# Optimization experiments

Hardware: AMD Instinct MI355X
Metric: run time of the kernel (lower is better)

Reference implementation:

```python
import jax, jax.numpy as jnp
import numpy as np

D_MODEL = 1024
N_HEADS = 16
HEAD_DIM = D_MODEL // N_HEADS
B, L, E = 2, 2048, 256


def _linear_params(key, d_out, d_in):
    kw, kb = jax.random.split(key)
    lim = 1.0 / np.sqrt(d_in)
    W = jax.random.uniform(kw, (d_out, d_in), jnp.float32, -lim, lim)
    b = jax.random.uniform(kb, (d_out,), jnp.float32, -lim, lim)
    return W, b


def setup_inputs() -> dict:
    key = jax.random.key(0)
    ks = jax.random.split(key, 10)
    x = jax.random.normal(ks[0], (B, L, D_MODEL), jnp.float32)
    kg_embeds = jax.random.normal(ks[1], (B, E, D_MODEL), jnp.float32)
    Wq, bq = _linear_params(ks[2], D_MODEL, D_MODEL)
    Wk, bk = _linear_params(ks[3], D_MODEL, D_MODEL)
    Wv, bv = _linear_params(ks[4], D_MODEL, D_MODEL)
    Wo, bo = _linear_params(ks[5], D_MODEL, D_MODEL)
    Wkk, bkk = _linear_params(ks[6], D_MODEL, D_MODEL)
    Wkv, bkv = _linear_params(ks[7], D_MODEL, D_MODEL)
    Wg, bg = _linear_params(ks[8], D_MODEL, 2 * D_MODEL)
    return {"x": x, "kg_embeds": kg_embeds,
            "Wq": Wq, "bq": bq, "Wk": Wk, "bk": bk, "Wv": Wv, "bv": bv,
            "Wkk": Wkk, "bkk": bkk, "Wkv": Wkv, "bkv": bkv,
            "Wo": Wo, "bo": bo, "Wg": Wg, "bg": bg}


def _heads(t):
    # [B, S, D] -> [B, H, S, hd]
    Bb, S, _ = t.shape
    return t.reshape(Bb, S, N_HEADS, HEAD_DIM).transpose(0, 2, 1, 3)


def reference(x, kg_embeds, Wq, bq, Wk, bk, Wv, bv, Wkk, bkk, Wkv, bkv, Wo, bo, Wg, bg):
    scale = HEAD_DIM ** -0.5
    q = _heads(x @ Wq.T + bq)                      # [B,H,L,hd]
    k = _heads(x @ Wk.T + bk)
    v = _heads(x @ Wv.T + bv)
    k_kg = _heads(kg_embeds @ Wkk.T + bkk)         # [B,H,E,hd]
    v_kg = _heads(kg_embeds @ Wkv.T + bkv)
    k_aug = jnp.concatenate([k, k_kg], axis=2)     # [B,H,L+E,hd]
    v_aug = jnp.concatenate([v, v_kg], axis=2)
    scores = jnp.einsum('bhld,bhmd->bhlm', q, k_aug) * scale  # [B,H,L,L+E]
    attn = jax.nn.softmax(scores, axis=-1)
    out = jnp.einsum('bhlm,bhmd->bhld', attn, v_aug)           # [B,H,L,hd]
    out = out.transpose(0, 2, 1, 3).reshape(x.shape)            # [B,L,D]
    kg_global = jnp.broadcast_to(kg_embeds.mean(axis=1, keepdims=True), x.shape)
    gate = jax.nn.sigmoid(jnp.concatenate([out, kg_global], axis=-1) @ Wg.T + bg)
    return gate * (out @ Wo.T + bo) + (1.0 - gate) * x
```

## Files before the change

### kernel.cpp

```cpp
#include <hip/hip_runtime.h>
#include <stdint.h>

typedef unsigned short ushort_t;
typedef __attribute__((ext_vector_type(8))) short short8;
typedef __attribute__((ext_vector_type(4))) short short4v;
typedef __attribute__((ext_vector_type(4))) float f32x4;
typedef __attribute__((ext_vector_type(4))) unsigned uintx4;

#define DEV static __device__ __forceinline__

DEV unsigned short f2bf(float f) {
  unsigned u = __builtin_bit_cast(unsigned, f);
  u += 0x7fffu + ((u >> 16) & 1u);
  return (unsigned short)(u >> 16);
}
DEV float bf2f(unsigned short b) {
  return __builtin_bit_cast(float, (unsigned)b << 16);
}

DEV void gl16(const void* g, void* l) {
  __builtin_amdgcn_global_load_lds(
      (__attribute__((address_space(1))) char*)(unsigned long long)g,
      (__attribute__((address_space(3))) char*)(unsigned)(unsigned long long)l,
      16, 0, 0);
}

DEV f32x4 mfma_bf16(short8 a, short8 b, f32x4 c) {
  return __builtin_amdgcn_mfma_f32_16x16x32_bf16(a, b, c, 0, 0, 0);
}

DEV unsigned cvtpk(float lo, float hi) {
  unsigned r;
  asm("v_cvt_pk_bf16_f32 %0, %1, %2" : "=v"(r) : "v"(lo), "v"(hi));
  return r;
}
DEV void swap_net(unsigned& a, unsigned& b) {
  asm("v_permlane32_swap_b32 %0, %1" : "+v"(a), "+v"(b));
  asm("v_permlane16_swap_b32 %0, %1" : "+v"(a), "+v"(b));
}
DEV float redmax4(float x) {
  unsigned a = __builtin_bit_cast(unsigned, x), b = a;
  asm("v_permlane16_swap_b32 %0, %1" : "+v"(a), "+v"(b));
  float y = fmaxf(__builtin_bit_cast(float, a), __builtin_bit_cast(float, b));
  unsigned c = __builtin_bit_cast(unsigned, y), d = c;
  asm("v_permlane32_swap_b32 %0, %1" : "+v"(c), "+v"(d));
  return fmaxf(__builtin_bit_cast(float, c), __builtin_bit_cast(float, d));
}
DEV float lanebcast(float v, int srclane) {
  return __builtin_bit_cast(float,
      __builtin_amdgcn_ds_bpermute(srclane * 4, __builtin_bit_cast(int, v)));
}

__global__ __launch_bounds__(256) void k_cvt_all(
    const float* __restrict__ x, const float* __restrict__ kg,
    const float* __restrict__ Wq, const float* __restrict__ Wk, const float* __restrict__ Wv,
    const float* __restrict__ Wkk, const float* __restrict__ Wkv,
    const float* __restrict__ Wo, const float* __restrict__ Wg,
    ushort_t* __restrict__ xh, ushort_t* __restrict__ kgh,
    ushort_t* __restrict__ WB1, ushort_t* __restrict__ WB2, ushort_t* __restrict__ WB3) {
  const int b = blockIdx.x;
  if (b >= 10752) {
    const int i = (b - 10752) * 256 + threadIdx.x;
    const int r = i >> 8, c = (i & 255) * 4;
    const float4 v = *(const float4*)(Wg + (size_t)r * 2048 + c);
    short4v o;
    o.x = (short)f2bf(v.x); o.y = (short)f2bf(v.y); o.z = (short)f2bf(v.z); o.w = (short)f2bf(v.w);
    *(short4v*)(WB3 + 1048576 + (size_t)r * 1024 + c) = o;
    return;
  }
  const float* src;
  ushort_t* dst;
  int off;
  if (b < 4096)       { src = x;   dst = xh;            off = b; }
  else if (b < 4608)  { src = kg;  dst = kgh;           off = b - 4096; }
  else if (b < 5632)  { src = Wq;  dst = WB1;           off = b - 4608; }
  else if (b < 6656)  { src = Wk;  dst = WB1 + 1048576; off = b - 5632; }
  else if (b < 7680)  { src = Wv;  dst = WB1 + 2097152; off = b - 6656; }
  else if (b < 8704)  { src = Wkk; dst = WB2;           off = b - 7680; }
  else if (b < 9728)  { src = Wkv; dst = WB2 + 1048576; off = b - 8704; }
  else                { src = Wo;  dst = WB3;           off = b - 9728; }
  const int i = off * 1024 + threadIdx.x * 4;
  const float4 v = *(const float4*)(src + i);
  short4v o;
  o.x = (short)f2bf(v.x); o.y = (short)f2bf(v.y); o.z = (short)f2bf(v.z); o.w = (short)f2bf(v.w);
  *(short4v*)(dst + i) = o;
}

__global__ __launch_bounds__(256) void k_kgmean(const float* __restrict__ kg, float* __restrict__ out) {
  const int i = blockIdx.x * 256 + threadIdx.x;
  const int b = i >> 10, d = i & 1023;
  float s = 0.f;
  #pragma unroll 4
  for (int e = 0; e < 256; e++) s += kg[((size_t)b * 256 + e) * 1024 + d];
  out[i] = s * (1.0f / 256.0f);
}

__global__ __launch_bounds__(256) void k_g2(const float* __restrict__ kgm, const float* __restrict__ Wg,
                                            const float* __restrict__ bg, float* __restrict__ g2) {
  const int w = threadIdx.x >> 6, l = threadIdx.x & 63;
  const int idx = blockIdx.x * 4 + w;
  const int b = idx >> 10, n = idx & 1023;
  const float* wr = Wg + (size_t)n * 2048 + 1024;
  const float* mb = kgm + b * 1024;
  float s = 0.f;
  #pragma unroll
  for (int j = 0; j < 16; j++) s += mb[j * 64 + l] * wr[j * 64 + l];
  #pragma unroll
  for (int m = 32; m >= 1; m >>= 1) s += __shfl_xor(s, m);
  if (l == 0) g2[idx] = s + bg[n];
}

template <int MODE>
__global__ __launch_bounds__(256, 3) void k_mm128(
    const ushort_t* __restrict__ A0, const ushort_t* __restrict__ B0,
    const ushort_t* __restrict__ A1, const ushort_t* __restrict__ B1,
    const float* __restrict__ f0, const float* __restrict__ f1, const float* __restrict__ f2,
    const float* __restrict__ f3, const float* __restrict__ f4,
    ushort_t* __restrict__ o0, ushort_t* __restrict__ o1, ushort_t* __restrict__ o2) {
  __shared__ __align__(16) char SHb[49152];
  const int tid = threadIdx.x;
  const int w = tid >> 6, l = tid & 63;
  const int wr = w >> 1, wc = w & 1;
  const int fr = l & 15, fg = l >> 4;

  int m0, n0, iskg = 0;
  if (MODE == 0) {
    const int wg = ((int)blockIdx.x & 7) * 104 + ((int)blockIdx.x >> 3);
    if (wg < 768) { m0 = (wg / 24) * 128; n0 = (wg % 24) * 128; }
    else          { const int k = wg - 768; iskg = 1; m0 = (k >> 4) * 128; n0 = (k & 15) * 128; }
  } else {
    const int wg = ((int)blockIdx.x & 7) * 64 + ((int)blockIdx.x >> 3);
    m0 = (wg >> 4) * 128; n0 = (wg & 15) * 128;
  }
  const ushort_t* A = (MODE == 0 && iskg) ? A1 : A0;
  const ushort_t* B = (MODE == 0 && iskg) ? B1 : B0;

  int grow[2], gcb[2];
  #pragma unroll
  for (int j = 0; j < 2; j++) {
    const int beta = j * 256 + tid;
    const int rp = beta >> 3;
    const int u = (beta & 7) ^ (rp & 7);
    grow[j] = 2 * rp + (u >> 2);
    gcb[j] = u & 3;
  }
  const char* gA[2];
  const char* gB[2];
  #pragma unroll
  for (int j = 0; j < 2; j++) {
    gA[j] = (const char*)A + (size_t)(m0 + grow[j]) * 2048 + gcb[j] * 16;
    gB[j] = (const char*)B + (size_t)(n0 + grow[j]) * 2048 + gcb[j] * 16;
  }

  auto stage = [&](int s, int kt) {
    char* As = SHb + s * 16384;
    char* Bs = As + 8192;
    const int ko = kt * 64;
    #pragma unroll
    for (int j = 0; j < 2; j++) {
      gl16(gA[j] + ko, As + j * 4096 + tid * 16);
      gl16(gB[j] + ko, Bs + j * 4096 + tid * 16);
    }
  };

  int aoff[4], boff[4];
  #pragma unroll
  for (int i = 0; i < 4; i++) {
    const int rowa = wr * 64 + i * 16 + fr;
    aoff[i] = (rowa >> 1) * 128 + ((((rowa & 1) << 6) | (fg << 4)) ^ (((rowa >> 1) & 7) << 4));
    const int rowb = wc * 64 + i * 16 + fr;
    boff[i] = (rowb >> 1) * 128 + ((((rowb & 1) << 6) | (fg << 4)) ^ (((rowb >> 1) & 7) << 4));
  }

  f32x4 acc[4][4] = {};

  stage(0, 0);
  stage(1, 1);
  int sc = 0, sn2 = 2;
  for (int kt = 0; kt < 32; kt++) {
    if (kt < 31) asm volatile("s_waitcnt vmcnt(4)" ::: "memory");
    else         asm volatile("s_waitcnt vmcnt(0)" ::: "memory");
    __builtin_amdgcn_s_barrier();
    asm volatile("" ::: "memory");
    if (kt < 30) stage(sn2, kt + 2);
    const char* Ab = SHb + sc * 16384;
    const char* Bb = Ab + 8192;
    short8 af[4], bf[4];
    #pragma unroll
    for (int j = 0; j < 4; j++) bf[j] = *(const short8*)(Bb + boff[j]);
    #pragma unroll
    for (int i = 0; i < 4; i++) af[i] = *(const short8*)(Ab + aoff[i]);
    __builtin_amdgcn_s_setprio(1);
    #pragma unroll
    for (int i = 0; i < 4; i++)
      #pragma unroll
      for (int j = 0; j < 4; j++)
        acc[i][j] = mfma_bf16(af[i], bf[j], acc[i][j]);
    __builtin_amdgcn_s_setprio(0);
    sc++; if (sc == 3) sc = 0;
    sn2++; if (sn2 == 3) sn2 = 0;
  }
  __syncthreads();

  const int sec = n0 >> 10;
  const bool isV = (MODE == 0) && ((!iskg && sec == 2) || (iskg && sec == 1));

  if (isV) {
    ushort_t* SHs = (ushort_t*)SHb;
    const float* bV = iskg ? f4 : f2;
    const int bidx = iskg ? (m0 >> 8) : (m0 >> 11);
    const int colbase = iskg ? (2048 + (m0 & 255)) : (m0 & 2047);
    #pragma unroll
    for (int i = 0; i < 4; i++) {
      #pragma unroll
      for (int j = 0; j < 4; j++) {
        const int nl = wc * 64 + j * 16 + fr;
        const int ml0 = wr * 64 + i * 16 + fg * 4;
        const float bb = bV[(n0 & 1023) + nl];
        short4v pk;
        #pragma unroll
        for (int r = 0; r < 4; r++) pk[r] = (short)f2bf(acc[i][j][r] + bb);
        *(short4v*)(SHs + nl * 128 + (ml0 ^ ((nl & 7) << 3))) = pk;
      }
    }
    __syncthreads();
    const int row = tid >> 1, half = tid & 1;
    const int h = ((n0 & 1023) >> 6) + (row >> 6);
    const int d = row & 63;
    ushort_t* dst = o2 + ((size_t)(bidx * 16 + h) * 64 + d) * 2304 + colbase + half * 64;
    const ushort_t* srow2 = SHs + row * 128;
    #pragma unroll
    for (int k2 = 0; k2 < 8; k2++) {
      const int me = (half * 64 + k2 * 8) ^ ((row & 7) << 3);
      *(short8*)(dst + k2 * 8) = *(const short8*)(srow2 + me);
    }
    return;
  }

  #pragma unroll
  for (int i = 0; i < 4; i++) {
    #pragma unroll
    for (int j = 0; j < 4; j++) {
      const int nn = (n0 & 1023) + wc * 64 + j * 16 + fr;
      const int h = nn >> 6, d = nn & 63;
      #pragma unroll
      for (int r = 0; r < 4; r++) {
        const int m = m0 + wr * 64 + i * 16 + fg * 4 + r;
        const float v = acc[i][j][r];
        if (MODE == 0) {
          if (iskg) {
            const int b = m >> 8, e = m & 255;
            o1[((size_t)(b * 16 + h) * 2304 + 2048 + e) * 64 + d] = f2bf(v + f3[nn]);
          } else if (sec == 0) {
            const int b = m >> 11, lq = m & 2047;
            o0[((size_t)(b * 16 + h) * 2048 + lq) * 64 + d] = f2bf((v + f0[nn]) * 0.18033688f);
          } else {
            const int b = m >> 11, lq = m & 2047;
            o1[((size_t)(b * 16 + h) * 2304 + lq) * 64 + d] = f2bf(v + f1[nn]);
          }
        } else {
          if (sec == 0) o0[(size_t)m * 1024 + nn] = f2bf(v + f0[nn]);
          else          o1[(size_t)m * 1024 + nn] = f2bf(v + f1[(m >> 11) * 1024 + nn]);
        }
      }
    }
  }
}

__global__ __launch_bounds__(256, 4) void k_attn(
    const ushort_t* __restrict__ Qg, const ushort_t* __restrict__ Kg,
    const ushort_t* __restrict__ Vtg, ushort_t* __restrict__ Og) {
  __shared__ __align__(16) ushort_t Ks[2][64 * 64];
  __shared__ __align__(16) ushort_t Vs[2][64 * 64];
  const int tid = threadIdx.x;
  const int w = tid >> 6, l = tid & 63;
  const int fr = l & 15, fg = l >> 4;

  const int id = blockIdx.y * gridDim.x + blockIdx.x;
  const int bh = (id & 7) * 4 + ((id >> 3) >> 5);
  const int q0 = ((id >> 3) & 31) * 64 + w * 16;

  short8 qf[2];
  {
    const short* qrow = (const short*)(Qg + ((size_t)bh * 2048 + q0 + fr) * 64);
    qf[0] = *(const short8*)(qrow + fg * 8);
    qf[1] = *(const short8*)(qrow + 32 + fg * 8);
  }

  constexpr short ONE = 0x3F80;
  const short8 ones = {ONE, ONE, ONE, ONE, ONE, ONE, ONE, ONE};

  f32x4 o[4] = {};
  f32x4 lacc = {};
  float mrun = -1.0e30f;

  const int rsub = tid >> 3;
  const int cS = ((tid & 7) * 16) ^ ((rsub & 7) << 4);
  const char* kbase = (const char*)(Kg + (size_t)bh * 2304 * 64);
  const char* vbase = (const char*)(Vtg + (size_t)bh * 64 * 2304);

  auto stage = [&](int nb, int tile) {
    #pragma unroll
    for (int j = 0; j < 2; j++) {
      const int row = j * 32 + rsub;
      gl16(kbase + (size_t)(tile * 64 + row) * 128 + cS,
           (char*)&Ks[nb][0] + j * 4096 + tid * 16);
      gl16(vbase + (size_t)row * 4608 + tile * 128 + cS,
           (char*)&Vs[nb][0] + j * 4096 + tid * 16);
    }
  };

  stage(0, 0);

  const int rswz = (fr & 7) << 4;

  for (int mt = 0; mt < 36; mt++) {
    __syncthreads();
    if (mt < 35) stage((mt + 1) & 1, mt + 1);

    const char* Kb = (const char*)&Ks[mt & 1][0];
    const char* Vb = (const char*)&Vs[mt & 1][0];

    f32x4 s[4];
    #pragma unroll
    for (int t = 0; t < 4; t++) {
      const int rb = (t * 16 + fr) * 128 + fg * 16;
      const short8 k0 = *(const short8*)(Kb + (rb ^ rswz));
      const short8 k1 = *(const short8*)(Kb + ((rb + 64) ^ rswz));
      f32x4 z = {};
      z = mfma_bf16(k0, qf[0], z);
      z = mfma_bf16(k1, qf[1], z);
      s[t] = z;
    }

    float m = s[0][0];
    #pragma unroll
    for (int t = 0; t < 4; t++)
      #pragma unroll
      for (int r = 0; r < 4; r++) m = fmaxf(m, s[t][r]);
    const float mx = redmax4(m);
    if (__any(mx - mrun > 11.5416f)) {
      const float mn = fmaxf(mrun, mx);
      const float al = __builtin_amdgcn_exp2f(mrun - mn);
      mrun = mn;
      float ab[4];
      #pragma unroll
      for (int r = 0; r < 4; r++) ab[r] = lanebcast(al, fg * 4 + r);
      #pragma unroll
      for (int r = 0; r < 4; r++) {
        lacc[r] *= ab[r];
        #pragma unroll
        for (int dt = 0; dt < 4; dt++) o[dt][r] *= ab[r];
      }
    }
    #pragma unroll
    for (int t = 0; t < 4; t++)
      #pragma unroll
      for (int r = 0; r < 4; r++)
        s[t][r] = __builtin_amdgcn_exp2f(s[t][r] - mrun);

    #pragma unroll
    for (int c = 0; c < 2; c++) {
      unsigned a0 = cvtpk(s[2 * c][0], s[2 * c][1]);
      unsigned b0 = cvtpk(s[2 * c + 1][0], s[2 * c + 1][1]);
      unsigned a1 = cvtpk(s[2 * c][2], s[2 * c][3]);
      unsigned b1 = cvtpk(s[2 * c + 1][2], s[2 * c + 1][3]);
      swap_net(a0, b0);
      swap_net(a1, b1);
      uintx4 u;
      u.x = a0; u.y = a1; u.z = b0; u.w = b1;
      const short8 pf = __builtin_bit_cast(short8, u);
      lacc = mfma_bf16(pf, ones, lacc);
      #pragma unroll
      for (int dt = 0; dt < 4; dt++) {
        const int vb2 = ((dt * 16 + fr) * 128) + fg * 16 + c * 64;
        const short8 vf = *(const short8*)(Vb + (vb2 ^ rswz));
        o[dt] = mfma_bf16(pf, vf, o[dt]);
      }
    }
  }

  const int b = bh >> 4, h = bh & 15;
  #pragma unroll
  for (int r = 0; r < 4; r++) {
    const float inv = 1.0f / lacc[r];
    const int q = q0 + fg * 4 + r;
    ushort_t* orow = Og + ((size_t)b * 2048 + q) * 1024 + h * 64;
    #pragma unroll
    for (int dt = 0; dt < 4; dt++) orow[dt * 16 + fr] = f2bf(o[dt][r] * inv);
  }
}

__global__ __launch_bounds__(256) void k_final(const float* __restrict__ x,
                                               const ushort_t* __restrict__ OUT,
                                               const ushort_t* __restrict__ GL,
                                               float* __restrict__ y) {
  const int i = (blockIdx.x * 256 + threadIdx.x) * 4;
  const float4 xv = *(const float4*)(x + i);
  const short4v ov = *(const short4v*)((const short*)OUT + i);
  const short4v gv = *(const short4v*)((const short*)GL + i);
  float4 r;
  {
    const float o0 = bf2f((unsigned short)ov.x);
    const float g0 = 1.f / (1.f + __expf(-bf2f((unsigned short)gv.x)));
    r.x = xv.x + g0 * (o0 - xv.x);
  }
  {
    const float o1 = bf2f((unsigned short)ov.y);
    const float g1 = 1.f / (1.f + __expf(-bf2f((unsigned short)gv.y)));
    r.y = xv.y + g1 * (o1 - xv.y);
  }
  {
    const float o2 = bf2f((unsigned short)ov.z);
    const float g2 = 1.f / (1.f + __expf(-bf2f((unsigned short)gv.z)));
    r.z = xv.z + g2 * (o2 - xv.z);
  }
  {
    const float o3 = bf2f((unsigned short)ov.w);
    const float g3 = 1.f / (1.f + __expf(-bf2f((unsigned short)gv.w)));
    r.w = xv.w + g3 * (o3 - xv.w);
  }
  *(float4*)(y + i) = r;
}

extern "C" void kernel_launch(void* const* d_in, const int* in_sizes, int n_in,
                              void* d_out, int out_size, void* d_ws, size_t ws_size,
                              hipStream_t stream) {
  (void)in_sizes; (void)n_in; (void)out_size; (void)ws_size;
  const float* x   = (const float*)d_in[0];
  const float* kg  = (const float*)d_in[1];
  const float* Wq  = (const float*)d_in[2];
  const float* bq  = (const float*)d_in[3];
  const float* Wk  = (const float*)d_in[4];
  const float* bk  = (const float*)d_in[5];
  const float* Wv  = (const float*)d_in[6];
  const float* bv  = (const float*)d_in[7];
  const float* Wkk = (const float*)d_in[8];
  const float* bkk = (const float*)d_in[9];
  const float* Wkv = (const float*)d_in[10];
  const float* bkv = (const float*)d_in[11];
  const float* Wo  = (const float*)d_in[12];
  const float* bo  = (const float*)d_in[13];
  const float* Wg  = (const float*)d_in[14];
  const float* bg  = (const float*)d_in[15];
  float* y = (float*)d_out;

  char* ws = (char*)d_ws;
  size_t off = 0;
  auto take = [&](size_t bytes) {
    char* p = ws + off;
    off += (bytes + 255) & ~(size_t)255;
    return p;
  };
  ushort_t* xh   = (ushort_t*)take((size_t)4096 * 1024 * 2);
  ushort_t* kgh  = (ushort_t*)take((size_t)512 * 1024 * 2);
  ushort_t* WB1  = (ushort_t*)take((size_t)3072 * 1024 * 2);
  ushort_t* WB2  = (ushort_t*)take((size_t)2048 * 1024 * 2);
  ushort_t* WB3  = (ushort_t*)take((size_t)2048 * 1024 * 2);
  ushort_t* Qg   = (ushort_t*)take((size_t)32 * 2048 * 64 * 2);
  ushort_t* Kaug = (ushort_t*)take((size_t)32 * 2304 * 64 * 2);
  ushort_t* Vt   = (ushort_t*)take((size_t)32 * 2304 * 64 * 2);
  ushort_t* Og   = (ushort_t*)take((size_t)4096 * 1024 * 2);
  ushort_t* OUTb = (ushort_t*)take((size_t)4096 * 1024 * 2);
  ushort_t* GLb  = (ushort_t*)take((size_t)4096 * 1024 * 2);
  float* kgm     = (float*)take(2048 * 4);
  float* g2      = (float*)take(2048 * 4);

  k_cvt_all<<<11776, 256, 0, stream>>>(x, kg, Wq, Wk, Wv, Wkk, Wkv, Wo, Wg,
                                       xh, kgh, WB1, WB2, WB3);
  k_kgmean<<<8, 256, 0, stream>>>(kg, kgm);
  k_g2<<<512, 256, 0, stream>>>(kgm, Wg, bg, g2);

  k_mm128<0><<<832, 256, 0, stream>>>(xh, WB1, kgh, WB2,
                                      bq, bk, bv, bkk, bkv, Qg, Kaug, Vt);
  k_attn<<<dim3(32, 32), 256, 0, stream>>>(Qg, Kaug, Vt, Og);
  k_mm128<1><<<512, 256, 0, stream>>>(Og, WB3, nullptr, nullptr,
                                      bo, g2, nullptr, nullptr, nullptr, OUTb, GLb, nullptr);
  k_final<<<4096, 256, 0, stream>>>(x, OUTb, GLb, y);
}
```

Before: 179.4 us.

## Fuse output and gate GEMMs with the sigmoid-blend epilogue into one kernel

Adds a dedicated output GEMM kernel in which each block computes a 64x128 tile against both Wo and the gate weights at once, sharing the A tile. The sigmoid gating and residual blend with x are applied in the epilogue and written straight to y. This drops the final elementwise kernel and the bf16 OUT/GL intermediate round trips through memory. The cost is more accumulator registers (occupancy target lowered to 2), plus a small reordering of the max reduction in attention.

```diff
diff --git a/kernel.cpp b/kernel.cpp
--- a/kernel.cpp
+++ b/kernel.cpp
@@ -110,7 +110,6 @@
   if (l == 0) g2[idx] = s + bg[n];
 }
 
-template <int MODE>
 __global__ __launch_bounds__(256, 3) void k_mm128(
     const ushort_t* __restrict__ A0, const ushort_t* __restrict__ B0,
     const ushort_t* __restrict__ A1, const ushort_t* __restrict__ B1,
@@ -124,16 +123,13 @@
   const int fr = l & 15, fg = l >> 4;
 
   int m0, n0, iskg = 0;
-  if (MODE == 0) {
+  {
     const int wg = ((int)blockIdx.x & 7) * 104 + ((int)blockIdx.x >> 3);
     if (wg < 768) { m0 = (wg / 24) * 128; n0 = (wg % 24) * 128; }
     else          { const int k = wg - 768; iskg = 1; m0 = (k >> 4) * 128; n0 = (k & 15) * 128; }
-  } else {
-    const int wg = ((int)blockIdx.x & 7) * 64 + ((int)blockIdx.x >> 3);
-    m0 = (wg >> 4) * 128; n0 = (wg & 15) * 128;
-  }
-  const ushort_t* A = (MODE == 0 && iskg) ? A1 : A0;
-  const ushort_t* B = (MODE == 0 && iskg) ? B1 : B0;
+  }
+  const ushort_t* A = iskg ? A1 : A0;
+  const ushort_t* B = iskg ? B1 : B0;
 
   int grow[2], gcb[2];
   #pragma unroll
@@ -203,7 +199,7 @@
   __syncthreads();
 
   const int sec = n0 >> 10;
-  const bool isV = (MODE == 0) && ((!iskg && sec == 2) || (iskg && sec == 1));
+  const bool isV = (!iskg && sec == 2) || (iskg && sec == 1);
 
   if (isV) {
     ushort_t* SHs = (ushort_t*)SHb;
@@ -247,21 +243,126 @@
       for (int r = 0; r < 4; r++) {
         const int m = m0 + wr * 64 + i * 16 + fg * 4 + r;
         const float v = acc[i][j][r];
-        if (MODE == 0) {
-          if (iskg) {
-            const int b = m >> 8, e = m & 255;
-            o1[((size_t)(b * 16 + h) * 2304 + 2048 + e) * 64 + d] = f2bf(v + f3[nn]);
-          } else if (sec == 0) {
-            const int b = m >> 11, lq = m & 2047;
-            o0[((size_t)(b * 16 + h) * 2048 + lq) * 64 + d] = f2bf((v + f0[nn]) * 0.18033688f);
-          } else {
-            const int b = m >> 11, lq = m & 2047;
-            o1[((size_t)(b * 16 + h) * 2304 + lq) * 64 + d] = f2bf(v + f1[nn]);
-          }
+        if (iskg) {
+          const int b = m >> 8, e = m & 255;
+          o1[((size_t)(b * 16 + h) * 2304 + 2048 + e) * 64 + d] = f2bf(v + f3[nn]);
+        } else if (sec == 0) {
+          const int b = m >> 11, lq = m & 2047;
+          o0[((size_t)(b * 16 + h) * 2048 + lq) * 64 + d] = f2bf((v + f0[nn]) * 0.18033688f);
         } else {
-          if (sec == 0) o0[(size_t)m * 1024 + nn] = f2bf(v + f0[nn]);
-          else          o1[(size_t)m * 1024 + nn] = f2bf(v + f1[(m >> 11) * 1024 + nn]);
+          const int b = m >> 11, lq = m & 2047;
+          o1[((size_t)(b * 16 + h) * 2304 + lq) * 64 + d] = f2bf(v + f1[nn]);
         }
+      }
+    }
+  }
+}
+
+__global__ __launch_bounds__(256, 2) void k_mmout(
+    const ushort_t* __restrict__ Og, const ushort_t* __restrict__ WB3,
+    const float* __restrict__ bo, const float* __restrict__ g2v,
+    const float* __restrict__ x, float* __restrict__ y) {
+  __shared__ __align__(16) char SHb[61440];
+  const int tid = threadIdx.x;
+  const int w = tid >> 6, l = tid & 63;
+  const int wr = w >> 1, wc = w & 1;
+  const int fr = l & 15, fg = l >> 4;
+
+  const int wg = ((int)blockIdx.x & 7) * 64 + ((int)blockIdx.x >> 3);
+  const int m0 = (wg >> 3) * 64, n0 = (wg & 7) * 128;
+
+  const int rpA = tid >> 3, uA = (tid & 7) ^ (rpA & 7);
+  const char* gAp = (const char*)Og + (size_t)(m0 + 2 * rpA + (uA >> 2)) * 2048 + (uA & 3) * 16;
+  int grow[2], gcb[2];
+  #pragma unroll
+  for (int j = 0; j < 2; j++) {
+    const int beta = j * 256 + tid;
+    const int rp = beta >> 3;
+    const int u = (beta & 7) ^ (rp & 7);
+    grow[j] = 2 * rp + (u >> 2);
+    gcb[j] = u & 3;
+  }
+  const char* gBo[2];
+  const char* gBg[2];
+  #pragma unroll
+  for (int j = 0; j < 2; j++) {
+    gBo[j] = (const char*)WB3 + (size_t)(n0 + grow[j]) * 2048 + gcb[j] * 16;
+    gBg[j] = (const char*)(WB3 + 1048576) + (size_t)(n0 + grow[j]) * 2048 + gcb[j] * 16;
+  }
+
+  auto stage = [&](int s, int kt) {
+    char* As = SHb + s * 20480;
+    const int ko = kt * 64;
+    gl16(gAp + ko, As + tid * 16);
+    #pragma unroll
+    for (int j = 0; j < 2; j++) {
+      gl16(gBo[j] + ko, As + 4096 + j * 4096 + tid * 16);
+      gl16(gBg[j] + ko, As + 12288 + j * 4096 + tid * 16);
+    }
+  };
+
+  int aoff[2], boff[4];
+  #pragma unroll
+  for (int i = 0; i < 2; i++) {
+    const int rowa = wr * 32 + i * 16 + fr;
+    aoff[i] = (rowa >> 1) * 128 + ((((rowa & 1) << 6) | (fg << 4)) ^ (((rowa >> 1) & 7) << 4));
+  }
+  #pragma unroll
+  for (int j = 0; j < 4; j++) {
+    const int rowb = wc * 64 + j * 16 + fr;
+    boff[j] = (rowb >> 1) * 128 + ((((rowb & 1) << 6) | (fg << 4)) ^ (((rowb >> 1) & 7) << 4));
+  }
+
+  f32x4 ao[2][4] = {};
+  f32x4 ag[2][4] = {};
+
+  stage(0, 0);
+  stage(1, 1);
+  int sc = 0, sn2 = 2;
+  for (int kt = 0; kt < 32; kt++) {
+    if (kt < 31) asm volatile("s_waitcnt vmcnt(5)" ::: "memory");
+    else         asm volatile("s_waitcnt vmcnt(0)" ::: "memory");
+    __builtin_amdgcn_s_barrier();
+    asm volatile("" ::: "memory");
+    if (kt < 30) stage(sn2, kt + 2);
+    const char* Ab = SHb + sc * 20480;
+    short8 af[2], bof[4], bgf[4];
+    #pragma unroll
+    for (int i = 0; i < 2; i++) af[i] = *(const short8*)(Ab + aoff[i]);
+    #pragma unroll
+    for (int j = 0; j < 4; j++) {
+      bof[j] = *(const short8*)(Ab + 4096 + boff[j]);
+      bgf[j] = *(const short8*)(Ab + 12288 + boff[j]);
+    }
+    __builtin_amdgcn_s_setprio(1);
+    #pragma unroll
+    for (int i = 0; i < 2; i++)
+      #pragma unroll
+      for (int j = 0; j < 4; j++) {
+        ao[i][j] = mfma_bf16(af[i], bof[j], ao[i][j]);
+        ag[i][j] = mfma_bf16(af[i], bgf[j], ag[i][j]);
+      }
+    __builtin_amdgcn_s_setprio(0);
+    sc++; if (sc == 3) sc = 0;
+    sn2++; if (sn2 == 3) sn2 = 0;
+  }
+
+  const int bidx = m0 >> 11;
+  #pragma unroll
+  for (int i = 0; i < 2; i++) {
+    #pragma unroll
+    for (int j = 0; j < 4; j++) {
+      const int nn = n0 + wc * 64 + j * 16 + fr;
+      const float bb = bo[nn];
+      const float gg = g2v[bidx * 1024 + nn];
+      #pragma unroll
+      for (int r = 0; r < 4; r++) {
+        const int m = m0 + wr * 32 + i * 16 + fg * 4 + r;
+        const float co = ao[i][j][r] + bb;
+        const float cg = ag[i][j][r] + gg;
+        const float gate = 1.0f / (1.0f + __builtin_amdgcn_exp2f(cg * -1.4426950408889634f));
+        const float xv = x[(size_t)m * 1024 + nn];
+        y[(size_t)m * 1024 + nn] = xv + gate * (co - xv);
       }
     }
   }
@@ -333,11 +434,14 @@
       s[t] = z;
     }
 
-    float m = s[0][0];
-    #pragma unroll
-    for (int t = 0; t < 4; t++)
-      #pragma unroll
-      for (int r = 0; r < 4; r++) m = fmaxf(m, s[t][r]);
+    float m = fmaxf(s[0][0], s[0][1]);
+    m = fmaxf(fmaxf(m, s[0][2]), s[0][3]);
+    m = fmaxf(fmaxf(m, s[1][0]), s[1][1]);
+    m = fmaxf(fmaxf(m, s[1][2]), s[1][3]);
+    m = fmaxf(fmaxf(m, s[2][0]), s[2][1]);
+    m = fmaxf(fmaxf(m, s[2][2]), s[2][3]);
+    m = fmaxf(fmaxf(m, s[3][0]), s[3][1]);
+    m = fmaxf(fmaxf(m, s[3][2]), s[3][3]);
     const float mx = redmax4(m);
     if (__any(mx - mrun > 11.5416f)) {
       const float mn = fmaxf(mrun, mx);
@@ -389,38 +493,6 @@
     #pragma unroll
     for (int dt = 0; dt < 4; dt++) orow[dt * 16 + fr] = f2bf(o[dt][r] * inv);
   }
-}
-
-__global__ __launch_bounds__(256) void k_final(const float* __restrict__ x,
-                                               const ushort_t* __restrict__ OUT,
-                                               const ushort_t* __restrict__ GL,
-                                               float* __restrict__ y) {
-  const int i = (blockIdx.x * 256 + threadIdx.x) * 4;
-  const float4 xv = *(const float4*)(x + i);
-  const short4v ov = *(const short4v*)((const short*)OUT + i);
-  const short4v gv = *(const short4v*)((const short*)GL + i);
-  float4 r;
-  {
-    const float o0 = bf2f((unsigned short)ov.x);
-    const float g0 = 1.f / (1.f + __expf(-bf2f((unsigned short)gv.x)));
-    r.x = xv.x + g0 * (o0 - xv.x);
-  }
-  {
-    const float o1 = bf2f((unsigned short)ov.y);
-    const float g1 = 1.f / (1.f + __expf(-bf2f((unsigned short)gv.y)));
-    r.y = xv.y + g1 * (o1 - xv.y);
-  }
-  {
-    const float o2 = bf2f((unsigned short)ov.z);
-    const float g2 = 1.f / (1.f + __expf(-bf2f((unsigned short)gv.z)));
-    r.z = xv.z + g2 * (o2 - xv.z);
-  }
-  {
-    const float o3 = bf2f((unsigned short)ov.w);
-    const float g3 = 1.f / (1.f + __expf(-bf2f((unsigned short)gv.w)));
-    r.w = xv.w + g3 * (o3 - xv.w);
-  }
-  *(float4*)(y + i) = r;
 }
 
 extern "C" void kernel_launch(void* const* d_in, const int* in_sizes, int n_in,
@@ -461,8 +533,6 @@
   ushort_t* Kaug = (ushort_t*)take((size_t)32 * 2304 * 64 * 2);
   ushort_t* Vt   = (ushort_t*)take((size_t)32 * 2304 * 64 * 2);
   ushort_t* Og   = (ushort_t*)take((size_t)4096 * 1024 * 2);
-  ushort_t* OUTb = (ushort_t*)take((size_t)4096 * 1024 * 2);
-  ushort_t* GLb  = (ushort_t*)take((size_t)4096 * 1024 * 2);
   float* kgm     = (float*)take(2048 * 4);
   float* g2      = (float*)take(2048 * 4);
 
@@ -471,10 +541,8 @@
   k_kgmean<<<8, 256, 0, stream>>>(kg, kgm);
   k_g2<<<512, 256, 0, stream>>>(kgm, Wg, bg, g2);
 
-  k_mm128<0><<<832, 256, 0, stream>>>(xh, WB1, kgh, WB2,
-                                      bq, bk, bv, bkk, bkv, Qg, Kaug, Vt);
+  k_mm128<<<832, 256, 0, stream>>>(xh, WB1, kgh, WB2,
+                                   bq, bk, bv, bkk, bkv, Qg, Kaug, Vt);
   k_attn<<<dim3(32, 32), 256, 0, stream>>>(Qg, Kaug, Vt, Og);
-  k_mm128<1><<<512, 256, 0, stream>>>(Og, WB3, nullptr, nullptr,
-                                      bo, g2, nullptr, nullptr, nullptr, OUTb, GLb, nullptr);
-  k_final<<<4096, 256, 0, stream>>>(x, OUTb, GLb, y);
-}
+  k_mmout<<<512, 256, 0, stream>>>(Og, WB3, bo, g2, x, y);
+}
```

Result: no change. 177.1 us (-1.3%).
